# Kernel tuning notes

Hardware: AMD Instinct MI355X
Metric: run time of the kernel (lower is better)

The kernel has to match this reference:

```python
import jax, jax.numpy as jnp
import numpy as np

DIM = 96
EPS = 1e-5

def setup_inputs() -> dict:
    key = jax.random.key(0)
    k1, k2, k3, k4 = jax.random.split(key, 4)
    x = jax.random.normal(k1, (2, DIM, 32, 64, 64), dtype=jnp.float32)
    # LayerNorm(8*dim) params and Linear(8*dim -> 2*dim, bias=False) weight
    gamma = jnp.ones((8 * DIM,), dtype=jnp.float32)
    beta = jnp.zeros((8 * DIM,), dtype=jnp.float32)
    w_red = jax.random.normal(k2, (8 * DIM, 2 * DIM), dtype=jnp.float32) * (1.0 / np.sqrt(8 * DIM))
    return {"x": x, "gamma": gamma, "beta": beta, "w_red": w_red}


def _patch_merge(x, gamma, beta, w_red):
    B, C, D, H, W = x.shape
    # pad trailing spatial dims to even (static shapes -> python ifs are fine)
    if (D % 2) or (H % 2) or (W % 2):
        x = jnp.pad(x, ((0, 0), (0, 0), (0, D % 2), (0, H % 2), (0, W % 2)))
    x = jnp.transpose(x, (0, 2, 3, 4, 1))  # B, D, H, W, C
    # gather the 8 octant sub-lattices and concat on channel
    parts = [x[:, d::2, h::2, w::2, :]
             for d in (0, 1) for h in (0, 1) for w in (0, 1)]
    # torch order: x0..x7 indexed by (d,h,w) bits with d slowest -> matches loop order
    y = jnp.concatenate(parts, axis=-1)  # B, D/2, H/2, W/2, 8C
    # LayerNorm over last dim
    mu = jnp.mean(y, axis=-1, keepdims=True)
    var = jnp.mean(jnp.square(y - mu), axis=-1, keepdims=True)
    y = (y - mu) * jax.lax.rsqrt(var + EPS) * gamma + beta
    # Linear 8C -> 2C, no bias
    y = jnp.einsum('bdhwc,co->bdhwo', y, w_red)
    return jnp.transpose(y, (0, 4, 1, 2, 3))  # B, 2C, D/2, H/2, W/2


def reference(x, gamma, beta, w_red):
    return _patch_merge(x, gamma, beta, w_red)
```

## Files before the change

kernel.cpp:

```cpp
#include <hip/hip_runtime.h>

typedef __attribute__((ext_vector_type(8))) short short8;
typedef __attribute__((ext_vector_type(4))) float float4v;
typedef __attribute__((ext_vector_type(4))) unsigned int uint4v;

__device__ __forceinline__ unsigned short f2bf(float f) {
  unsigned int u = __float_as_uint(f);
  u += 0x7fffu + ((u >> 16) & 1u);
  return (unsigned short)(u >> 16);
}
__device__ __forceinline__ float bf2f(unsigned short h) {
  return __uint_as_float(((unsigned int)h) << 16);
}

__global__ __launch_bounds__(256, 2)
void pm_kernel(const float* __restrict__ x, const float* __restrict__ gamma,
               const float* __restrict__ beta, const float* __restrict__ w_red,
               float* __restrict__ out) {
  __shared__ __align__(16) unsigned short Y[32][776];
  __shared__ __align__(16) unsigned short Bs[192][40];
  __shared__ float gammaP[768];
  __shared__ float betaP[768];

  const int tid = threadIdx.x;
  const int bid = blockIdx.x;
  const int b  = bid >> 9;
  const int dz = (bid >> 5) & 15;
  const int hy = bid & 31;

  const float* xb = x + (size_t)b * 12582912u + (size_t)dz * 8192u + (size_t)hy * 128u;

  for (int t = tid; t < 768; t += 256) {
    int ko = (t & 7) * 96 + (t >> 3);
    gammaP[t] = gamma[ko];
    betaP[t]  = beta[ko];
  }

#pragma unroll
  for (int it = 0; it < 24; ++it) {
    int idx4 = it * 256 + tid;
    int r  = idx4 >> 4;
    int c  = r >> 2;
    int di = (r >> 1) & 1;
    int hi = r & 1;
    int w0 = (idx4 & 15) << 2;
    float4 v = *(const float4*)(xb + (size_t)c * 131072u + di * 4096 + hi * 64 + w0);
    int wx0 = (idx4 & 15) << 1;
    int k0  = c * 8 + di * 4 + hi * 2;
    unsigned int p01 = (unsigned int)f2bf(v.x) | ((unsigned int)f2bf(v.y) << 16);
    unsigned int p23 = (unsigned int)f2bf(v.z) | ((unsigned int)f2bf(v.w) << 16);
    *(unsigned int*)&Y[wx0][k0]     = p01;
    *(unsigned int*)&Y[wx0 + 1][k0] = p23;
  }
  __syncthreads();

  const int m   = tid >> 3;
  const int sub = tid & 7;
  float sum = 0.f, sq = 0.f;
  short8 vals[12];
#pragma unroll
  for (int j = 0; j < 12; ++j) {
    short8 v = *(const short8*)&Y[m][sub * 96 + j * 8];
    vals[j] = v;
#pragma unroll
    for (int e = 0; e < 8; ++e) {
      float f = bf2f((unsigned short)v[e]);
      sum += f; sq += f * f;
    }
  }
#pragma unroll
  for (int off = 1; off < 8; off <<= 1) {
    sum += __shfl_xor(sum, off, 64);
    sq  += __shfl_xor(sq,  off, 64);
  }
  const float mu  = sum * (1.f / 768.f);
  const float var = sq * (1.f / 768.f) - mu * mu;
  const float rs  = rsqrtf(var + 1e-5f);

#pragma unroll
  for (int j = 0; j < 12; ++j) {
    int kp = sub * 96 + j * 8;
    short8 v = vals[j];
    short8 o;
#pragma unroll
    for (int e = 0; e < 8; ++e) {
      float f  = bf2f((unsigned short)v[e]);
      float nv = (f - mu) * rs * gammaP[kp + e] + betaP[kp + e];
      o[e] = (short)f2bf(nv);
    }
    *(short8*)&Y[m][kp] = o;
  }
  __syncthreads();

  const int lane = tid & 63;
  const int wave = tid >> 6;
  const int lrow = lane & 15;
  const int lq   = lane >> 4;

  float4v acc[2][3];
#pragma unroll
  for (int i2 = 0; i2 < 2; ++i2)
#pragma unroll
    for (int j2 = 0; j2 < 3; ++j2)
#pragma unroll
      for (int r = 0; r < 4; ++r) acc[i2][j2][r] = 0.f;

  for (int kc = 0; kc < 24; ++kc) {
    if (kc) __syncthreads();
#pragma unroll
    for (int it = 0; it < 3; ++it) {
      int id = it * 256 + tid;
      int qb = id / 192;
      int n  = id - qb * 192;
      const float* wp = w_red + (size_t)(kc * 4 + qb) * 192 + n;
      uint4v pk;
#pragma unroll
      for (int jj = 0; jj < 4; ++jj) {
        float a0 = wp[(size_t)(2 * jj)     * 18432];
        float a1 = wp[(size_t)(2 * jj + 1) * 18432];
        pk[jj] = (unsigned int)f2bf(a0) | ((unsigned int)f2bf(a1) << 16);
      }
      *(uint4v*)&Bs[n][qb * 8] = pk;
    }
    __syncthreads();

    short8 a0 = *(const short8*)&Y[lrow][kc * 32 + lq * 8];
    short8 a1 = *(const short8*)&Y[16 + lrow][kc * 32 + lq * 8];
#pragma unroll
    for (int t3 = 0; t3 < 3; ++t3) {
      int nt = wave * 3 + t3;
      short8 bf = *(const short8*)&Bs[nt * 16 + lrow][lq * 8];
      acc[0][t3] = __builtin_amdgcn_mfma_f32_16x16x32_bf16(a0, bf, acc[0][t3], 0, 0, 0);
      acc[1][t3] = __builtin_amdgcn_mfma_f32_16x16x32_bf16(a1, bf, acc[1][t3], 0, 0, 0);
    }
  }

  __syncthreads();
  float* Cs = (float*)&Y[0][0];
#pragma unroll
  for (int mt = 0; mt < 2; ++mt)
#pragma unroll
    for (int t3 = 0; t3 < 3; ++t3) {
      int ng = (wave * 3 + t3) * 16 + lrow;
#pragma unroll
      for (int r = 0; r < 4; ++r) {
        Cs[ng * 40 + mt * 16 + lq * 4 + r] = acc[mt][t3][r];
      }
    }
  __syncthreads();

  float* ob = out + (size_t)b * 3145728u + (size_t)dz * 1024u + (size_t)hy * 32u;
#pragma unroll
  for (int it = 0; it < 6; ++it) {
    int idx4 = it * 256 + tid;
    int o  = idx4 >> 3;
    int wq = idx4 & 7;
    float4 vv = *(const float4*)&Cs[o * 40 + wq * 4];
    *(float4*)(ob + (size_t)o * 16384u + wq * 4) = vv;
  }
}

extern "C" void kernel_launch(void* const* d_in, const int* in_sizes, int n_in,
                              void* d_out, int out_size, void* d_ws, size_t ws_size,
                              hipStream_t stream) {
  const float* x     = (const float*)d_in[0];
  const float* gamma = (const float*)d_in[1];
  const float* beta  = (const float*)d_in[2];
  const float* w_red = (const float*)d_in[3];
  float* out = (float*)d_out;
  pm_kernel<<<dim3(1024), dim3(256), 0, stream>>>(x, gamma, beta, w_red, out);
}
```

Measured before the change: 212.4 us.

## Fold LayerNorm affine into pre-converted bf16 weights and apply stats post-GEMM

```diff
diff --git a/kernel.cpp b/kernel.cpp
--- a/kernel.cpp
+++ b/kernel.cpp
@@ -2,7 +2,6 @@
 
 typedef __attribute__((ext_vector_type(8))) short short8;
 typedef __attribute__((ext_vector_type(4))) float float4v;
-typedef __attribute__((ext_vector_type(4))) unsigned int uint4v;
 
 __device__ __forceinline__ unsigned short f2bf(float f) {
   unsigned int u = __float_as_uint(f);
@@ -13,14 +12,45 @@
   return __uint_as_float(((unsigned int)h) << 16);
 }
 
-__global__ __launch_bounds__(256, 2)
-void pm_kernel(const float* __restrict__ x, const float* __restrict__ gamma,
-               const float* __restrict__ beta, const float* __restrict__ w_red,
+__global__ __launch_bounds__(256)
+void prep_kernel(const float* __restrict__ w_red, const float* __restrict__ gamma,
+                 const float* __restrict__ beta, unsigned short* __restrict__ w_bf,
+                 float* __restrict__ colsum, float* __restrict__ bias) {
+  const int n = blockIdx.x;
+  const int t = threadIdx.x;
+  float cs = 0.f, bs = 0.f;
+#pragma unroll
+  for (int j = 0; j < 3; ++j) {
+    int kp = j * 256 + t;
+    int ko = (kp & 7) * 96 + (kp >> 3);
+    float w = w_red[(size_t)ko * 192 + n];
+    unsigned short v = f2bf(gamma[ko] * w);
+    w_bf[(size_t)n * 768 + kp] = v;
+    cs += bf2f(v);
+    bs += beta[ko] * w;
+  }
+#pragma unroll
+  for (int off = 1; off < 64; off <<= 1) {
+    cs += __shfl_xor(cs, off, 64);
+    bs += __shfl_xor(bs, off, 64);
+  }
+  __shared__ float red[2][4];
+  const int wave = t >> 6;
+  if ((t & 63) == 0) { red[0][wave] = cs; red[1][wave] = bs; }
+  __syncthreads();
+  if (t == 0) {
+    colsum[n] = red[0][0] + red[0][1] + red[0][2] + red[0][3];
+    bias[n]   = red[1][0] + red[1][1] + red[1][2] + red[1][3];
+  }
+}
+
+__global__ __launch_bounds__(256, 3)
+void pm_kernel(const float* __restrict__ x, const unsigned short* __restrict__ w_bf,
+               const float* __restrict__ colsum, const float* __restrict__ bias,
                float* __restrict__ out) {
   __shared__ __align__(16) unsigned short Y[32][776];
-  __shared__ __align__(16) unsigned short Bs[192][40];
-  __shared__ float gammaP[768];
-  __shared__ float betaP[768];
+  __shared__ float4 part4[4][16];
+  __shared__ float smu[32], srs[32];
 
   const int tid = threadIdx.x;
   const int bid = blockIdx.x;
@@ -30,12 +60,7 @@
 
   const float* xb = x + (size_t)b * 12582912u + (size_t)dz * 8192u + (size_t)hy * 128u;
 
-  for (int t = tid; t < 768; t += 256) {
-    int ko = (t & 7) * 96 + (t >> 3);
-    gammaP[t] = gamma[ko];
-    betaP[t]  = beta[ko];
-  }
-
+  float sum0 = 0.f, sq0 = 0.f, sum1 = 0.f, sq1 = 0.f;
 #pragma unroll
   for (int it = 0; it < 24; ++it) {
     int idx4 = it * 256 + tid;
@@ -51,49 +76,34 @@
     unsigned int p23 = (unsigned int)f2bf(v.z) | ((unsigned int)f2bf(v.w) << 16);
     *(unsigned int*)&Y[wx0][k0]     = p01;
     *(unsigned int*)&Y[wx0 + 1][k0] = p23;
+    sum0 += v.x + v.y;  sq0 += v.x * v.x + v.y * v.y;
+    sum1 += v.z + v.w;  sq1 += v.z * v.z + v.w * v.w;
   }
+#pragma unroll
+  for (int off = 16; off < 64; off <<= 1) {
+    sum0 += __shfl_xor(sum0, off, 64);  sq0 += __shfl_xor(sq0, off, 64);
+    sum1 += __shfl_xor(sum1, off, 64);  sq1 += __shfl_xor(sq1, off, 64);
+  }
+  const int lane = tid & 63;
+  const int wave = tid >> 6;
+  if (lane < 16) part4[wave][lane] = make_float4(sum0, sq0, sum1, sq1);
   __syncthreads();
 
-  const int m   = tid >> 3;
-  const int sub = tid & 7;
-  float sum = 0.f, sq = 0.f;
-  short8 vals[12];
+  if (tid < 32) {
+    int sp = tid >> 1, odd = tid & 1;
+    float s = 0.f, q = 0.f;
 #pragma unroll
-  for (int j = 0; j < 12; ++j) {
-    short8 v = *(const short8*)&Y[m][sub * 96 + j * 8];
-    vals[j] = v;
-#pragma unroll
-    for (int e = 0; e < 8; ++e) {
-      float f = bf2f((unsigned short)v[e]);
-      sum += f; sq += f * f;
+    for (int w = 0; w < 4; ++w) {
+      float4 p = part4[w][sp];
+      s += odd ? p.z : p.x;
+      q += odd ? p.w : p.y;
     }
+    float mu  = s * (1.f / 768.f);
+    float var = q * (1.f / 768.f) - mu * mu;
+    smu[tid] = mu;
+    srs[tid] = rsqrtf(var + 1e-5f);
   }
-#pragma unroll
-  for (int off = 1; off < 8; off <<= 1) {
-    sum += __shfl_xor(sum, off, 64);
-    sq  += __shfl_xor(sq,  off, 64);
-  }
-  const float mu  = sum * (1.f / 768.f);
-  const float var = sq * (1.f / 768.f) - mu * mu;
-  const float rs  = rsqrtf(var + 1e-5f);
 
-#pragma unroll
-  for (int j = 0; j < 12; ++j) {
-    int kp = sub * 96 + j * 8;
-    short8 v = vals[j];
-    short8 o;
-#pragma unroll
-    for (int e = 0; e < 8; ++e) {
-      float f  = bf2f((unsigned short)v[e]);
-      float nv = (f - mu) * rs * gammaP[kp + e] + betaP[kp + e];
-      o[e] = (short)f2bf(nv);
-    }
-    *(short8*)&Y[m][kp] = o;
-  }
-  __syncthreads();
-
-  const int lane = tid & 63;
-  const int wave = tid >> 6;
   const int lrow = lane & 15;
   const int lq   = lane >> 4;
 
@@ -105,48 +115,47 @@
 #pragma unroll
       for (int r = 0; r < 4; ++r) acc[i2][j2][r] = 0.f;
 
+  const unsigned short* wrow[3];
+#pragma unroll
+  for (int t3 = 0; t3 < 3; ++t3)
+    wrow[t3] = w_bf + (size_t)((wave * 3 + t3) * 16 + lrow) * 768 + lq * 8;
+
+  short8 bcur[3];
+#pragma unroll
+  for (int t3 = 0; t3 < 3; ++t3) bcur[t3] = *(const short8*)(wrow[t3]);
+
   for (int kc = 0; kc < 24; ++kc) {
-    if (kc) __syncthreads();
+    int kn = (kc < 23) ? kc + 1 : kc;
+    short8 bnext[3];
 #pragma unroll
-    for (int it = 0; it < 3; ++it) {
-      int id = it * 256 + tid;
-      int qb = id / 192;
-      int n  = id - qb * 192;
-      const float* wp = w_red + (size_t)(kc * 4 + qb) * 192 + n;
-      uint4v pk;
-#pragma unroll
-      for (int jj = 0; jj < 4; ++jj) {
-        float a0 = wp[(size_t)(2 * jj)     * 18432];
-        float a1 = wp[(size_t)(2 * jj + 1) * 18432];
-        pk[jj] = (unsigned int)f2bf(a0) | ((unsigned int)f2bf(a1) << 16);
-      }
-      *(uint4v*)&Bs[n][qb * 8] = pk;
-    }
-    __syncthreads();
-
+    for (int t3 = 0; t3 < 3; ++t3) bnext[t3] = *(const short8*)(wrow[t3] + kn * 32);
     short8 a0 = *(const short8*)&Y[lrow][kc * 32 + lq * 8];
     short8 a1 = *(const short8*)&Y[16 + lrow][kc * 32 + lq * 8];
 #pragma unroll
     for (int t3 = 0; t3 < 3; ++t3) {
-      int nt = wave * 3 + t3;
-      short8 bf = *(const short8*)&Bs[nt * 16 + lrow][lq * 8];
-      acc[0][t3] = __builtin_amdgcn_mfma_f32_16x16x32_bf16(a0, bf, acc[0][t3], 0, 0, 0);
-      acc[1][t3] = __builtin_amdgcn_mfma_f32_16x16x32_bf16(a1, bf, acc[1][t3], 0, 0, 0);
+      acc[0][t3] = __builtin_amdgcn_mfma_f32_16x16x32_bf16(a0, bcur[t3], acc[0][t3], 0, 0, 0);
+      acc[1][t3] = __builtin_amdgcn_mfma_f32_16x16x32_bf16(a1, bcur[t3], acc[1][t3], 0, 0, 0);
     }
+#pragma unroll
+    for (int t3 = 0; t3 < 3; ++t3) bcur[t3] = bnext[t3];
   }
 
   __syncthreads();
   float* Cs = (float*)&Y[0][0];
 #pragma unroll
-  for (int mt = 0; mt < 2; ++mt)
+  for (int t3 = 0; t3 < 3; ++t3) {
+    int ng = (wave * 3 + t3) * 16 + lrow;
+    float cs_n = colsum[ng];
+    float bi_n = bias[ng];
 #pragma unroll
-    for (int t3 = 0; t3 < 3; ++t3) {
-      int ng = (wave * 3 + t3) * 16 + lrow;
+    for (int mt = 0; mt < 2; ++mt)
 #pragma unroll
       for (int r = 0; r < 4; ++r) {
-        Cs[ng * 40 + mt * 16 + lq * 4 + r] = acc[mt][t3][r];
+        int m = mt * 16 + lq * 4 + r;
+        float v = srs[m] * (acc[mt][t3][r] - smu[m] * cs_n) + bi_n;
+        Cs[ng * 40 + m] = v;
       }
-    }
+  }
   __syncthreads();
 
   float* ob = out + (size_t)b * 3145728u + (size_t)dz * 1024u + (size_t)hy * 32u;
@@ -168,5 +177,11 @@
   const float* beta  = (const float*)d_in[2];
   const float* w_red = (const float*)d_in[3];
   float* out = (float*)d_out;
-  pm_kernel<<<dim3(1024), dim3(256), 0, stream>>>(x, gamma, beta, w_red, out);
+
+  unsigned short* w_bf = (unsigned short*)d_ws;
+  float* colsum = (float*)((char*)d_ws + 294912);
+  float* bias   = colsum + 192;
+
+  prep_kernel<<<dim3(192), dim3(256), 0, stream>>>(w_red, gamma, beta, w_bf, colsum, bias);
+  pm_kernel<<<dim3(1024), dim3(256), 0, stream>>>(x, w_bf, colsum, bias, out);
 }
```

Result: faster. 204.6 us (-3.7%).
